# Optimization experiments

Hardware: AMD Instinct MI355X
Metric: run time of the kernel (lower is better)

The kernel has to match this reference:

```python
import jax, jax.numpy as jnp
import numpy as np

N_ATOMS = 50000
N_EDGES = 800000
EMB = 128      # emb_size_atom
EMB_BF = 128   # emb_size_bf
N_HIDDEN = 3
INV_SQRT2 = 0.7071067811865476
SILU_SCALE = 1.0 / 0.6  # GemNet ScaledSiLU


def scaled_silu(x):
    return jax.nn.silu(x) * SILU_SCALE


def residual_layer(x, w0, w1):
    # ResidualLayer(units, nLayers=2): two bias-free Dense+ScaledSiLU, then inv_sqrt(2)*(x + y)
    y = scaled_silu(x @ w0)
    y = scaled_silu(y @ w1)
    return (x + y) * INV_SQRT2


def setup_inputs() -> dict:
    key = jax.random.key(0)
    ks = jax.random.split(key, 9)
    s_emb = 1.0 / np.float32(np.sqrt(EMB))
    s_bf = 1.0 / np.float32(np.sqrt(EMB_BF))
    return {
        "h": jax.random.normal(ks[0], (N_ATOMS, EMB), jnp.float32),
        "bf": jax.random.uniform(ks[1], (N_EDGES, EMB_BF), jnp.float32),
        "idx_s": jax.random.randint(ks[2], (N_EDGES,), 0, N_ATOMS, jnp.int64),
        "idx_t": jax.random.randint(ks[3], (N_EDGES,), 0, N_ATOMS, jnp.int64),
        "w_bf": jax.random.normal(ks[4], (EMB_BF, EMB), jnp.float32) * s_bf,
        "w_pre": jax.random.normal(ks[5], (2, EMB, EMB), jnp.float32) * s_emb,
        "w_mlp1": jax.random.normal(ks[6], (EMB, EMB), jnp.float32) * s_emb,
        "w_res": jax.random.normal(ks[7], (N_HIDDEN, 2, EMB, EMB), jnp.float32) * s_emb,
        "scale_sum": jnp.ones((1,), jnp.float32),  # ScalingFactor (1.0 without scale_file)
    }


def reference(h, bf, idx_s, idx_t, w_bf, w_pre, w_mlp1, w_res, scale_sum):
    # pre_residual
    h_res = residual_layer(h, w_pre[0], w_pre[1])          # (nAtoms, EMB)
    # dense_bf: bias-free linear, no activation
    mlp_bf = bf @ w_bf                                     # (nEdges, EMB)
    # gather source embeddings, Hadamard multiply with edge features
    x = h_res[idx_s] * mlp_bf                              # (nEdges, EMB)
    # scatter-sum over target atoms
    x2 = jax.ops.segment_sum(x, idx_t, num_segments=N_ATOMS)  # (nAtoms, EMB)
    x = x2 * scale_sum[0]
    # MLP: Dense+activation, then nHidden residual blocks
    x = scaled_silu(x @ w_mlp1)
    for i in range(N_HIDDEN):
        x = residual_layer(x, w_res[i, 0], w_res[i, 1])
    return x
```

## Files before the change

### kernel.cpp

```cpp
#include <hip/hip_runtime.h>

#define EMB 128
#define NATOMS 50000
#define NEDGES 800000
#define PADN 50176

typedef __attribute__((ext_vector_type(8))) short bf16x8;
typedef __attribute__((ext_vector_type(4))) float f32x4;
typedef __attribute__((ext_vector_type(4))) unsigned short u16x4;

static const size_t H_RES_OFF  = 0;
static const size_t X2_OFF     = (size_t)NATOMS * EMB * 2;
static const size_t W_OFF      = X2_OFF + (size_t)NATOMS * EMB * 4;
static const size_t FLAG_OFF   = W_OFF + 10 * 128 * 128 * 2;
static const size_t COUNTS_OFF = (FLAG_OFF + 4 + 255) & ~(size_t)255;
static const size_t SEG_OFF    = COUNTS_OFF + (size_t)PADN * 4;
static const size_t CURSOR_OFF = SEG_OFF + (size_t)PADN * 4;
static const size_t BSUM_OFF   = CURSOR_OFF + (size_t)PADN * 4;
static const size_t RECS_OFF   = (BSUM_OFF + 1024 + 255) & ~(size_t)255;

__device__ __forceinline__ short f2bf(float f) {
  unsigned u = __float_as_uint(f);
  u += 0x7fffu + ((u >> 16) & 1u);
  return (short)(u >> 16);
}

__device__ __forceinline__ float bf2f(unsigned short u) {
  return __uint_as_float((unsigned)u << 16);
}

__device__ __forceinline__ float ssilu(float x) {
  return x * (1.0f / 0.6f) / (1.0f + __expf(-x));
}

__device__ __forceinline__ int xidx(int row, int k) {
  return (row << 7) + ((((k >> 2) ^ (row & 7)) << 2) | (k & 3));
}
__device__ __forceinline__ int bidx(int row, int k) {
  return (row << 7) + ((((k >> 3) ^ (row & 7)) << 3) | (k & 7));
}

__device__ __forceinline__ void stage_w(const short* __restrict__ src, short* dst) {
  const int wave = threadIdx.x >> 6;
  const int lane = threadIdx.x & 63;
  const char* s = (const char*)src;
  char* d = (char*)dst;
#pragma unroll
  for (int i = 0; i < 8; ++i) {
    const int off = wave * 8192 + i * 1024;
    __builtin_amdgcn_global_load_lds(
        (const __attribute__((address_space(1))) void*)(s + off + lane * 16),
        (__attribute__((address_space(3))) void*)(d + off), 16, 0, 0);
  }
}

__device__ __forceinline__ void stage_x(const float* __restrict__ src, int row0, float* x) {
#pragma unroll
  for (int i = 0; i < 8; ++i) {
    const int c = threadIdx.x + i * 256;
    const int row = c >> 5, unit = c & 31;
    f32x4 v = {0.f, 0.f, 0.f, 0.f};
    if (row0 + row < NATOMS) v = *(const f32x4*)(src + (size_t)(row0 + row) * EMB + unit * 4);
    *(f32x4*)&x[(row << 7) + ((unit ^ (row & 7)) << 2)] = v;
  }
}

template <bool SRC_BF16>
__device__ __forceinline__ void gemm_stage(const float* xsrc, const short* ysrc,
                                           const short* w, int wr0, int lr, int lh,
                                           f32x4* acc) {
#pragma unroll
  for (int kk = 0; kk < 4; ++kk) {
    const int k0 = kk * 32 + lh * 8;
    const int ra = wr0 + lr;
    bf16x8 a;
    if constexpr (SRC_BF16) {
      a = *(const bf16x8*)&ysrc[bidx(ra, k0)];
    } else {
      f32x4 u0 = *(const f32x4*)&xsrc[xidx(ra, k0)];
      f32x4 u1 = *(const f32x4*)&xsrc[xidx(ra, k0 + 4)];
      a[0] = f2bf(u0[0]); a[1] = f2bf(u0[1]); a[2] = f2bf(u0[2]); a[3] = f2bf(u0[3]);
      a[4] = f2bf(u1[0]); a[5] = f2bf(u1[1]); a[6] = f2bf(u1[2]); a[7] = f2bf(u1[3]);
    }
#pragma unroll
    for (int j0 = 0; j0 < 8; ++j0) {
      bf16x8 b = *(const bf16x8*)&w[bidx(j0 * 16 + lr, k0)];
      acc[j0] = __builtin_amdgcn_mfma_f32_16x16x32_bf16(a, b, acc[j0], 0, 0, 0);
    }
  }
}

__global__ void prep_weights(const float* __restrict__ wbf, const float* __restrict__ wpre,
                             const float* __restrict__ wmlp1, const float* __restrict__ wres,
                             short* __restrict__ W) {
  const int s = blockIdx.x >> 7;
  const int k = blockIdx.x & 127;
  const int n = threadIdx.x;
  const float* src;
  if (s == 0) src = wbf;
  else if (s <= 2) src = wpre + (s - 1) * 16384;
  else if (s == 3) src = wmlp1;
  else src = wres + (s - 4) * 16384;
  const float v = src[k * EMB + n];
  W[s * 16384 + (n << 7) + ((((k >> 3) ^ (n & 7)) << 3) | (k & 7))] = f2bf(v);
}

__global__ void zero_ws(float* __restrict__ x2, float* __restrict__ counts) {
  const f32x4 z = {0.f, 0.f, 0.f, 0.f};
  const int stride = gridDim.x * 256;
  const int nx = NATOMS * EMB / 4;
  for (int v = blockIdx.x * 256 + threadIdx.x; v < nx; v += stride)
    *(f32x4*)(x2 + 4 * (size_t)v) = z;
  const int nc = PADN / 4;
  for (int v = blockIdx.x * 256 + threadIdx.x; v < nc; v += stride)
    *(f32x4*)(counts + 4 * (size_t)v) = z;
}

__global__ void detect_idx(const int* __restrict__ idx, int* __restrict__ flag) {
  const int lane = threadIdx.x & 63;
  const int v = idx[2 * lane + 1];
  const unsigned long long nz = __ballot(v != 0);
  if (lane == 0) *flag = (nz == 0ull) ? 1 : 0;
}

__device__ __forceinline__ int load_idx(const void* p, int e, int f64) {
  return f64 ? (int)((const long long*)p)[e] : ((const int*)p)[e];
}

__global__ void hist_kernel(const void* __restrict__ idx_t_p, int* __restrict__ counts,
                            const int* __restrict__ flag) {
  const int e = blockIdx.x * 256 + threadIdx.x;
  if (e < NEDGES) atomicAdd(&counts[load_idx(idx_t_p, e, *flag)], 1);
}

__global__ void scan_blocks(const int* __restrict__ counts, int* __restrict__ seg,
                            int* __restrict__ bsum) {
  const int i = blockIdx.x * 256 + threadIdx.x;
  const int lane = threadIdx.x & 63, wave = threadIdx.x >> 6;
  const int v = counts[i];
  int incl = v;
#pragma unroll
  for (int d = 1; d < 64; d <<= 1) {
    int t = __shfl_up(incl, d, 64);
    if (lane >= d) incl += t;
  }
  __shared__ int wtot[4];
  if (lane == 63) wtot[wave] = incl;
  __syncthreads();
  int woff = 0;
  for (int w = 0; w < wave; ++w) woff += wtot[w];
  seg[i] = woff + incl - v;
  if (threadIdx.x == 255) bsum[blockIdx.x] = woff + incl;
}

__global__ void scan_top(int* __restrict__ bsum) {
  const int i = threadIdx.x;
  const int lane = i & 63, wave = i >> 6;
  const int v = (i < 196) ? bsum[i] : 0;
  int incl = v;
#pragma unroll
  for (int d = 1; d < 64; d <<= 1) {
    int t = __shfl_up(incl, d, 64);
    if (lane >= d) incl += t;
  }
  __shared__ int wtot[4];
  if (lane == 63) wtot[wave] = incl;
  __syncthreads();
  int woff = 0;
  for (int w = 0; w < wave; ++w) woff += wtot[w];
  if (i < 196) bsum[i] = woff + incl - v;
}

__global__ void add_off(int* __restrict__ seg, const int* __restrict__ bsum,
                        int* __restrict__ cursor) {
  const int i = blockIdx.x * 256 + threadIdx.x;
  const int s = seg[i] + bsum[blockIdx.x];
  seg[i] = s;
  cursor[i] = s;
}

__global__ void scatter_kernel(const void* __restrict__ idx_s_p, const void* __restrict__ idx_t_p,
                               int* __restrict__ cursor, int4* __restrict__ recs,
                               const int* __restrict__ flag) {
  const int e = blockIdx.x * 256 + threadIdx.x;
  if (e < NEDGES) {
    const int f64 = *flag;
    const int t = load_idx(idx_t_p, e, f64);
    const int s = load_idx(idx_s_p, e, f64);
    const int pos = atomicAdd(&cursor[t], 1);
    recs[pos] = make_int4(e, s, t, 0);
  }
}

__global__ __launch_bounds__(256, 2) void atom_pre(const float* __restrict__ h,
                                                   unsigned short* __restrict__ h_res,
                                                   const short* __restrict__ W) {
  __shared__ float x_lds[64 * 128];
  __shared__ short y_lds[64 * 128];
  __shared__ short w_lds[128 * 128];
  const int lane = threadIdx.x & 63, wave = threadIdx.x >> 6;
  const int lr = lane & 15, lh = lane >> 4;
  const int row0 = blockIdx.x * 64, wr0 = wave * 16;
  const f32x4 vzero = {0.f, 0.f, 0.f, 0.f};

  stage_x(h, row0, x_lds);
  stage_w(W + 1 * 16384, w_lds);
  __syncthreads();

  f32x4 acc[8];
#pragma unroll
  for (int j = 0; j < 8; ++j) acc[j] = vzero;
  gemm_stage<false>(x_lds, nullptr, w_lds, wr0, lr, lh, acc);
#pragma unroll
  for (int j0 = 0; j0 < 8; ++j0)
#pragma unroll
    for (int j = 0; j < 4; ++j)
      y_lds[bidx(wr0 + lh * 4 + j, j0 * 16 + lr)] = f2bf(ssilu(acc[j0][j]));

  __syncthreads();
  stage_w(W + 2 * 16384, w_lds);
  __syncthreads();

#pragma unroll
  for (int j = 0; j < 8; ++j) acc[j] = vzero;
  gemm_stage<true>(nullptr, y_lds, w_lds, wr0, lr, lh, acc);

#pragma unroll
  for (int j = 0; j < 4; ++j) {
    const int row = wr0 + lh * 4 + j;
    const int ga = row0 + row;
    if (ga < NATOMS) {
#pragma unroll
      for (int j0 = 0; j0 < 8; ++j0) {
        const int col = j0 * 16 + lr;
        h_res[(size_t)ga * EMB + col] = (unsigned short)f2bf(
            (x_lds[xidx(row, col)] + ssilu(acc[j0][j])) * 0.70710678118654752440f);
      }
    }
  }
}

__global__ __launch_bounds__(256, 4) void edge_swapped(const float* __restrict__ bf,
                                                       const unsigned short* __restrict__ h_res,
                                                       const int4* __restrict__ recs,
                                                       const short* __restrict__ W,
                                                       float* __restrict__ x2) {
  __shared__ short w_lds[128 * 128];
  const int lane = threadIdx.x & 63, wave = threadIdx.x >> 6;
  const int lr = lane & 15, lh = lane >> 4;

  stage_w(W, w_lds);

  const int p0 = blockIdx.x * 128 + wave * 32;
  const int4 rec = recs[p0 + (lane & 31)];
  const int it_mine = rec.z;

  const int eB0 = __shfl(rec.x, lr, 64);
  const int eB1 = __shfl(rec.x, 16 + lr, 64);
  const int isE0 = __shfl(rec.y, lr, 64);
  const int isE1 = __shfl(rec.y, 16 + lr, 64);

  __syncthreads();

  bf16x8 b_all[2][4];
#pragma unroll
  for (int kk = 0; kk < 4; ++kk) {
#pragma unroll
    for (int rf = 0; rf < 2; ++rf) {
      const int e = rf ? eB1 : eB0;
      const f32x4* p = (const f32x4*)(bf + (size_t)e * EMB + kk * 32 + lh * 8);
      f32x4 u0 = __builtin_nontemporal_load(p);
      f32x4 u1 = __builtin_nontemporal_load(p + 1);
      bf16x8 b;
      b[0] = f2bf(u0[0]); b[1] = f2bf(u0[1]); b[2] = f2bf(u0[2]); b[3] = f2bf(u0[3]);
      b[4] = f2bf(u1[0]); b[5] = f2bf(u1[1]); b[6] = f2bf(u1[2]); b[7] = f2bf(u1[3]);
      b_all[rf][kk] = b;
    }
  }

  const f32x4 vzero = {0.f, 0.f, 0.f, 0.f};

#pragma unroll 1
  for (int hf = 0; hf < 2; ++hf) {
    f32x4 acc[2][4];
#pragma unroll
    for (int rf = 0; rf < 2; ++rf)
#pragma unroll
      for (int q = 0; q < 4; ++q) acc[rf][q] = vzero;

#pragma unroll
    for (int kk = 0; kk < 4; ++kk) {
#pragma unroll
      for (int q = 0; q < 4; ++q) {
        bf16x8 a = *(const bf16x8*)&w_lds[bidx((4 * hf + q) * 16 + lr, kk * 32 + lh * 8)];
        acc[0][q] = __builtin_amdgcn_mfma_f32_16x16x32_bf16(a, b_all[0][kk], acc[0][q], 0, 0, 0);
        acc[1][q] = __builtin_amdgcn_mfma_f32_16x16x32_bf16(a, b_all[1][kk], acc[1][q], 0, 0, 0);
      }
    }

#pragma unroll
    for (int rf = 0; rf < 2; ++rf) {
      const unsigned short* hr = h_res + (size_t)(rf ? isE1 : isE0) * EMB + 4 * lh;
#pragma unroll
      for (int q = 0; q < 4; ++q) {
        u16x4 hv = *(const u16x4*)(hr + 16 * (4 * hf + q));
#pragma unroll
        for (int j = 0; j < 4; ++j) acc[rf][q][j] *= bf2f(hv[j]);
      }
    }

    int r = 0;
    while (r < 32) {
      const int t = __shfl(it_mine, r, 64);
      const unsigned long long bal = __ballot(it_mine == t);
      const unsigned long long m = (bal & 0xffffffffull) >> r;
      const int cnt = (int)__builtin_ctzll(~m);
      const int end = r + cnt;

      float v[4][4];
      const bool in0 = (lr >= r) && (lr < end);
      const bool in1 = (lr + 16 >= r) && (lr + 16 < end);
#pragma unroll
      for (int q = 0; q < 4; ++q)
#pragma unroll
        for (int j = 0; j < 4; ++j) {
          float s = 0.f;
          if (in0) s += acc[0][q][j];
          if (in1) s += acc[1][q][j];
          v[q][j] = s;
        }
#pragma unroll
      for (int d = 1; d < 16; d <<= 1)
#pragma unroll
        for (int q = 0; q < 4; ++q)
#pragma unroll
          for (int j = 0; j < 4; ++j)
            v[q][j] += __shfl_xor(v[q][j], d, 64);

      const bool interior = (r > 0) && (end < 32);
      if (lr == 0) {
        float* orow = x2 + (size_t)t * EMB + 4 * lh;
        if (interior) {
#pragma unroll
          for (int q = 0; q < 4; ++q) {
            f32x4 o = {v[q][0], v[q][1], v[q][2], v[q][3]};
            *(f32x4*)(orow + 16 * (4 * hf + q)) = o;
          }
        } else {
#pragma unroll
          for (int q = 0; q < 4; ++q)
#pragma unroll
            for (int j = 0; j < 4; ++j)
              atomicAdd(&orow[16 * (4 * hf + q) + j], v[q][j]);
        }
      }
      r = end;
    }
  }
}

__global__ __launch_bounds__(256, 2) void atom_post(const float* __restrict__ x2,
                                                    float* __restrict__ out,
                                                    const short* __restrict__ W,
                                                    const float* __restrict__ scale_sum) {
  __shared__ float x_lds[64 * 128];
  __shared__ short y_lds[64 * 128];
  __shared__ short w_lds[128 * 128];
  const int lane = threadIdx.x & 63, wave = threadIdx.x >> 6;
  const int lr = lane & 15, lh = lane >> 4;
  const int row0 = blockIdx.x * 64, wr0 = wave * 16;
  const float sc = scale_sum[0];
  const f32x4 vzero = {0.f, 0.f, 0.f, 0.f};

  stage_x(x2, row0, x_lds);
  stage_w(W + 3 * 16384, w_lds);
  __syncthreads();

  f32x4 acc[8];
#pragma unroll
  for (int j = 0; j < 8; ++j) acc[j] = vzero;
  gemm_stage<false>(x_lds, nullptr, w_lds, wr0, lr, lh, acc);
#pragma unroll
  for (int j0 = 0; j0 < 8; ++j0)
#pragma unroll
    for (int j = 0; j < 4; ++j)
      x_lds[xidx(wr0 + lh * 4 + j, j0 * 16 + lr)] = ssilu(acc[j0][j] * sc);

  for (int L = 0; L < 3; ++L) {
    __syncthreads();
    stage_w(W + (size_t)(4 + 2 * L) * 16384, w_lds);
    __syncthreads();
#pragma unroll
    for (int j = 0; j < 8; ++j) acc[j] = vzero;
    gemm_stage<false>(x_lds, nullptr, w_lds, wr0, lr, lh, acc);
#pragma unroll
    for (int j0 = 0; j0 < 8; ++j0)
#pragma unroll
      for (int j = 0; j < 4; ++j)
        y_lds[bidx(wr0 + lh * 4 + j, j0 * 16 + lr)] = f2bf(ssilu(acc[j0][j]));

    __syncthreads();
    stage_w(W + (size_t)(5 + 2 * L) * 16384, w_lds);
    __syncthreads();
#pragma unroll
    for (int j = 0; j < 8; ++j) acc[j] = vzero;
    gemm_stage<true>(nullptr, y_lds, w_lds, wr0, lr, lh, acc);

    if (L < 2) {
#pragma unroll
      for (int j = 0; j < 4; ++j) {
        const int row = wr0 + lh * 4 + j;
#pragma unroll
        for (int j0 = 0; j0 < 8; ++j0) {
          const int col = j0 * 16 + lr;
          const float xv = x_lds[xidx(row, col)];
          x_lds[xidx(row, col)] = (xv + ssilu(acc[j0][j])) * 0.70710678118654752440f;
        }
      }
    } else {
#pragma unroll
      for (int j = 0; j < 4; ++j) {
        const int row = wr0 + lh * 4 + j;
        const int ga = row0 + row;
        if (ga < NATOMS) {
#pragma unroll
          for (int j0 = 0; j0 < 8; ++j0) {
            const int col = j0 * 16 + lr;
            out[(size_t)ga * EMB + col] =
                (x_lds[xidx(row, col)] + ssilu(acc[j0][j])) * 0.70710678118654752440f;
          }
        }
      }
    }
  }
}

extern "C" void kernel_launch(void* const* d_in, const int* in_sizes, int n_in,
                              void* d_out, int out_size, void* d_ws, size_t ws_size,
                              hipStream_t stream) {
  const float* h      = (const float*)d_in[0];
  const float* bf     = (const float*)d_in[1];
  const void*  idx_s  = d_in[2];
  const void*  idx_t  = d_in[3];
  const float* w_bf   = (const float*)d_in[4];
  const float* w_pre  = (const float*)d_in[5];
  const float* w_mlp1 = (const float*)d_in[6];
  const float* w_res  = (const float*)d_in[7];
  const float* scale  = (const float*)d_in[8];
  float* out = (float*)d_out;

  char* ws = (char*)d_ws;
  unsigned short* h_res = (unsigned short*)(ws + H_RES_OFF);
  float* x2     = (float*)(ws + X2_OFF);
  short* W      = (short*)(ws + W_OFF);
  int*   flag   = (int*)(ws + FLAG_OFF);
  int*   counts = (int*)(ws + COUNTS_OFF);
  int*   segp   = (int*)(ws + SEG_OFF);
  int*   cursor = (int*)(ws + CURSOR_OFF);
  int*   bsum   = (int*)(ws + BSUM_OFF);
  int4*  recs   = (int4*)(ws + RECS_OFF);

  zero_ws<<<dim3(1024), dim3(256), 0, stream>>>(x2, (float*)counts);
  prep_weights<<<dim3(10 * 128), dim3(128), 0, stream>>>(w_bf, w_pre, w_mlp1, w_res, W);
  detect_idx<<<dim3(1), dim3(64), 0, stream>>>((const int*)idx_s, flag);

  hist_kernel<<<dim3(NEDGES / 256), dim3(256), 0, stream>>>(idx_t, counts, flag);
  scan_blocks<<<dim3(PADN / 256), dim3(256), 0, stream>>>(counts, segp, bsum);
  scan_top<<<dim3(1), dim3(256), 0, stream>>>(bsum);
  add_off<<<dim3(PADN / 256), dim3(256), 0, stream>>>(segp, bsum, cursor);
  scatter_kernel<<<dim3(NEDGES / 256), dim3(256), 0, stream>>>(idx_s, idx_t, cursor, recs, flag);

  atom_pre<<<dim3((NATOMS + 63) / 64), dim3(256), 0, stream>>>(h, h_res, W);
  edge_swapped<<<dim3(NEDGES / 128), dim3(256), 0, stream>>>(bf, h_res, recs, W, x2);
  atom_post<<<dim3((NATOMS + 63) / 64), dim3(256), 0, stream>>>(x2, out, W, scale);
}
```

Measured before the change: 366.9 us.

## Pack edge records to 8 bytes, read weights from global, prefetch h_res gathers

Edge records shrink from int4 to uint2 by packing source and target atom indices into 16 bits each, halving record traffic in the scatter and edge kernels. The edge kernel no longer stages the 128x128 weight tile into LDS or synchronises, and instead reads fragments directly from global memory, relying on cache. The h_res gathers are hoisted ahead of the MFMA loop to overlap their latency, and the half loop is fully unrolled. Register pressure rises and weight reads now depend on L1/L2 hit rates rather than LDS.

```diff
diff --git a/kernel.cpp b/kernel.cpp
--- a/kernel.cpp
+++ b/kernel.cpp
@@ -180,7 +180,7 @@
 }
 
 __global__ void scatter_kernel(const void* __restrict__ idx_s_p, const void* __restrict__ idx_t_p,
-                               int* __restrict__ cursor, int4* __restrict__ recs,
+                               int* __restrict__ cursor, uint2* __restrict__ recs,
                                const int* __restrict__ flag) {
   const int e = blockIdx.x * 256 + threadIdx.x;
   if (e < NEDGES) {
@@ -188,7 +188,7 @@
     const int t = load_idx(idx_t_p, e, f64);
     const int s = load_idx(idx_s_p, e, f64);
     const int pos = atomicAdd(&cursor[t], 1);
-    recs[pos] = make_int4(e, s, t, 0);
+    recs[pos] = make_uint2((unsigned)e, (unsigned)s | ((unsigned)t << 16));
   }
 }
 
@@ -240,27 +240,35 @@
   }
 }
 
-__global__ __launch_bounds__(256, 4) void edge_swapped(const float* __restrict__ bf,
-                                                       const unsigned short* __restrict__ h_res,
-                                                       const int4* __restrict__ recs,
-                                                       const short* __restrict__ W,
-                                                       float* __restrict__ x2) {
-  __shared__ short w_lds[128 * 128];
-  const int lane = threadIdx.x & 63, wave = threadIdx.x >> 6;
+__global__ __launch_bounds__(256) void edge_swapped(const float* __restrict__ bf,
+                                                    const unsigned short* __restrict__ h_res,
+                                                    const uint2* __restrict__ recs,
+                                                    const short* __restrict__ W,
+                                                    float* __restrict__ x2) {
+  const int lane = threadIdx.x & 63;
+  const int wave = threadIdx.x >> 6;
   const int lr = lane & 15, lh = lane >> 4;
 
-  stage_w(W, w_lds);
-
   const int p0 = blockIdx.x * 128 + wave * 32;
-  const int4 rec = recs[p0 + (lane & 31)];
-  const int it_mine = rec.z;
-
-  const int eB0 = __shfl(rec.x, lr, 64);
-  const int eB1 = __shfl(rec.x, 16 + lr, 64);
-  const int isE0 = __shfl(rec.y, lr, 64);
-  const int isE1 = __shfl(rec.y, 16 + lr, 64);
-
-  __syncthreads();
+  const uint2 rec = recs[p0 + (lane & 31)];
+  const int it_mine = (int)(rec.y >> 16);
+  const int is_mine = (int)(rec.y & 0xffffu);
+
+  const int eB0 = __shfl((int)rec.x, lr, 64);
+  const int eB1 = __shfl((int)rec.x, 16 + lr, 64);
+  const int isE0 = __shfl(is_mine, lr, 64);
+  const int isE1 = __shfl(is_mine, 16 + lr, 64);
+
+  u16x4 hv[2][2][4];
+#pragma unroll
+  for (int rf = 0; rf < 2; ++rf) {
+    const unsigned short* hr = h_res + (size_t)(rf ? isE1 : isE0) * EMB + 4 * lh;
+#pragma unroll
+    for (int hf = 0; hf < 2; ++hf)
+#pragma unroll
+      for (int q = 0; q < 4; ++q)
+        hv[rf][hf][q] = *(const u16x4*)(hr + 16 * (4 * hf + q));
+  }
 
   bf16x8 b_all[2][4];
 #pragma unroll
@@ -280,7 +288,7 @@
 
   const f32x4 vzero = {0.f, 0.f, 0.f, 0.f};
 
-#pragma unroll 1
+#pragma unroll
   for (int hf = 0; hf < 2; ++hf) {
     f32x4 acc[2][4];
 #pragma unroll
@@ -292,22 +300,19 @@
     for (int kk = 0; kk < 4; ++kk) {
 #pragma unroll
       for (int q = 0; q < 4; ++q) {
-        bf16x8 a = *(const bf16x8*)&w_lds[bidx((4 * hf + q) * 16 + lr, kk * 32 + lh * 8)];
+        bf16x8 a = *(const bf16x8*)&W[bidx((4 * hf + q) * 16 + lr, kk * 32 + lh * 8)];
         acc[0][q] = __builtin_amdgcn_mfma_f32_16x16x32_bf16(a, b_all[0][kk], acc[0][q], 0, 0, 0);
         acc[1][q] = __builtin_amdgcn_mfma_f32_16x16x32_bf16(a, b_all[1][kk], acc[1][q], 0, 0, 0);
       }
     }
 
 #pragma unroll
-    for (int rf = 0; rf < 2; ++rf) {
-      const unsigned short* hr = h_res + (size_t)(rf ? isE1 : isE0) * EMB + 4 * lh;
-#pragma unroll
-      for (int q = 0; q < 4; ++q) {
-        u16x4 hv = *(const u16x4*)(hr + 16 * (4 * hf + q));
-#pragma unroll
-        for (int j = 0; j < 4; ++j) acc[rf][q][j] *= bf2f(hv[j]);
-      }
-    }
+    for (int rf = 0; rf < 2; ++rf)
+#pragma unroll
+      for (int q = 0; q < 4; ++q)
+#pragma unroll
+        for (int j = 0; j < 4; ++j)
+          acc[rf][q][j] *= bf2f(hv[rf][hf][q][j]);
 
     int r = 0;
     while (r < 32) {
@@ -458,7 +463,7 @@
   int*   segp   = (int*)(ws + SEG_OFF);
   int*   cursor = (int*)(ws + CURSOR_OFF);
   int*   bsum   = (int*)(ws + BSUM_OFF);
-  int4*  recs   = (int4*)(ws + RECS_OFF);
+  uint2* recs   = (uint2*)(ws + RECS_OFF);
 
   zero_ws<<<dim3(1024), dim3(256), 0, stream>>>(x2, (float*)counts);
   prep_weights<<<dim3(10 * 128), dim3(128), 0, stream>>>(w_bf, w_pre, w_mlp1, w_res, W);
```

Measured after the change: 408.3 us. 11.3% more time.

## Split edge kernel into coalesced GEMM with sorted bf16 scatter and segment reduce

Applied to the files above, without the earlier changes.

The fused edge kernel, which gathered bf rows in sorted-target order, is split in two. A GEMM kernel reads bf coalesced in original edge order and writes bf16 results to their sorted positions through a per-edge rank array. A separate kernel then does the h_res gather, the multiply and the segmented reduction over contiguous sorted rows. Edge records are also packed into 32-bit words. This trades the scattered fp32 bf reads for an extra bf16 intermediate written and read back (about 200MB) plus a second launch.

```diff
diff --git a/kernel.cpp b/kernel.cpp
--- a/kernel.cpp
+++ b/kernel.cpp
@@ -8,6 +8,7 @@
 typedef __attribute__((ext_vector_type(8))) short bf16x8;
 typedef __attribute__((ext_vector_type(4))) float f32x4;
 typedef __attribute__((ext_vector_type(4))) unsigned short u16x4;
+typedef __attribute__((ext_vector_type(8))) unsigned short u16x8;
 
 static const size_t H_RES_OFF  = 0;
 static const size_t X2_OFF     = (size_t)NATOMS * EMB * 2;
@@ -17,7 +18,9 @@
 static const size_t SEG_OFF    = COUNTS_OFF + (size_t)PADN * 4;
 static const size_t CURSOR_OFF = SEG_OFF + (size_t)PADN * 4;
 static const size_t BSUM_OFF   = CURSOR_OFF + (size_t)PADN * 4;
-static const size_t RECS_OFF   = (BSUM_OFF + 1024 + 255) & ~(size_t)255;
+static const size_t RANK_OFF   = (BSUM_OFF + 1024 + 255) & ~(size_t)255;
+static const size_t RECS_OFF   = RANK_OFF + (size_t)NEDGES * 4;
+static const size_t MLP_OFF    = (RECS_OFF + (size_t)NEDGES * 4 + 255) & ~(size_t)255;
 
 __device__ __forceinline__ short f2bf(float f) {
   unsigned u = __float_as_uint(f);
@@ -180,15 +183,16 @@
 }
 
 __global__ void scatter_kernel(const void* __restrict__ idx_s_p, const void* __restrict__ idx_t_p,
-                               int* __restrict__ cursor, int4* __restrict__ recs,
-                               const int* __restrict__ flag) {
+                               int* __restrict__ cursor, int* __restrict__ rank,
+                               unsigned* __restrict__ recs, const int* __restrict__ flag) {
   const int e = blockIdx.x * 256 + threadIdx.x;
   if (e < NEDGES) {
     const int f64 = *flag;
     const int t = load_idx(idx_t_p, e, f64);
     const int s = load_idx(idx_s_p, e, f64);
     const int pos = atomicAdd(&cursor[t], 1);
-    recs[pos] = make_int4(e, s, t, 0);
+    rank[e] = pos;
+    recs[pos] = (unsigned)s | ((unsigned)t << 16);
   }
 }
 
@@ -240,35 +244,26 @@
   }
 }
 
-__global__ __launch_bounds__(256, 4) void edge_swapped(const float* __restrict__ bf,
-                                                       const unsigned short* __restrict__ h_res,
-                                                       const int4* __restrict__ recs,
-                                                       const short* __restrict__ W,
-                                                       float* __restrict__ x2) {
+__global__ __launch_bounds__(256, 2) void mlp_gemm(const float* __restrict__ bf,
+                                                   const int* __restrict__ rank,
+                                                   const short* __restrict__ W,
+                                                   unsigned short* __restrict__ mlp_s) {
   __shared__ short w_lds[128 * 128];
-  const int lane = threadIdx.x & 63, wave = threadIdx.x >> 6;
+  __shared__ unsigned short tile[128 * 128];
+  const int tid = threadIdx.x;
+  const int lane = tid & 63, wave = tid >> 6;
   const int lr = lane & 15, lh = lane >> 4;
+  const int ebase = blockIdx.x * 128;
+  const int e0 = ebase + wave * 32;
 
   stage_w(W, w_lds);
 
-  const int p0 = blockIdx.x * 128 + wave * 32;
-  const int4 rec = recs[p0 + (lane & 31)];
-  const int it_mine = rec.z;
-
-  const int eB0 = __shfl(rec.x, lr, 64);
-  const int eB1 = __shfl(rec.x, 16 + lr, 64);
-  const int isE0 = __shfl(rec.y, lr, 64);
-  const int isE1 = __shfl(rec.y, 16 + lr, 64);
-
-  __syncthreads();
-
   bf16x8 b_all[2][4];
 #pragma unroll
   for (int kk = 0; kk < 4; ++kk) {
 #pragma unroll
     for (int rf = 0; rf < 2; ++rf) {
-      const int e = rf ? eB1 : eB0;
-      const f32x4* p = (const f32x4*)(bf + (size_t)e * EMB + kk * 32 + lh * 8);
+      const f32x4* p = (const f32x4*)(bf + (size_t)(e0 + rf * 16 + lr) * EMB + kk * 32 + lh * 8);
       f32x4 u0 = __builtin_nontemporal_load(p);
       f32x4 u1 = __builtin_nontemporal_load(p + 1);
       bf16x8 b;
@@ -278,9 +273,10 @@
     }
   }
 
+  __syncthreads();
+
   const f32x4 vzero = {0.f, 0.f, 0.f, 0.f};
-
-#pragma unroll 1
+#pragma unroll
   for (int hf = 0; hf < 2; ++hf) {
     f32x4 acc[2][4];
 #pragma unroll
@@ -300,63 +296,109 @@
 
 #pragma unroll
     for (int rf = 0; rf < 2; ++rf) {
-      const unsigned short* hr = h_res + (size_t)(rf ? isE1 : isE0) * EMB + 4 * lh;
 #pragma unroll
       for (int q = 0; q < 4; ++q) {
-        u16x4 hv = *(const u16x4*)(hr + 16 * (4 * hf + q));
-#pragma unroll
-        for (int j = 0; j < 4; ++j) acc[rf][q][j] *= bf2f(hv[j]);
+        const int row = wave * 32 + rf * 16 + lr;
+        const int n0 = (4 * hf + q) * 16 + 4 * lh;
+        u16x4 pk;
+        pk[0] = (unsigned short)f2bf(acc[rf][q][0]);
+        pk[1] = (unsigned short)f2bf(acc[rf][q][1]);
+        pk[2] = (unsigned short)f2bf(acc[rf][q][2]);
+        pk[3] = (unsigned short)f2bf(acc[rf][q][3]);
+        *(u16x4*)&tile[(row << 7) + ((((n0 >> 3) ^ (row & 7)) << 3) | (n0 & 7))] = pk;
       }
     }
-
-    int r = 0;
-    while (r < 32) {
-      const int t = __shfl(it_mine, r, 64);
-      const unsigned long long bal = __ballot(it_mine == t);
-      const unsigned long long m = (bal & 0xffffffffull) >> r;
-      const int cnt = (int)__builtin_ctzll(~m);
-      const int end = r + cnt;
-
-      float v[4][4];
-      const bool in0 = (lr >= r) && (lr < end);
-      const bool in1 = (lr + 16 >= r) && (lr + 16 < end);
-#pragma unroll
-      for (int q = 0; q < 4; ++q)
-#pragma unroll
-        for (int j = 0; j < 4; ++j) {
-          float s = 0.f;
-          if (in0) s += acc[0][q][j];
-          if (in1) s += acc[1][q][j];
-          v[q][j] = s;
+  }
+
+  __syncthreads();
+
+#pragma unroll
+  for (int it = 0; it < 8; ++it) {
+    const int row = it * 16 + (tid >> 4);
+    const int unit = tid & 15;
+    const int pos = rank[ebase + row];
+    u16x8 v = *(const u16x8*)&tile[(row << 7) + ((unit ^ (row & 7)) << 3)];
+    __builtin_nontemporal_store(v, (u16x8*)(mlp_s + (size_t)pos * EMB + unit * 8));
+  }
+}
+
+__device__ __forceinline__ void seg_flush(float (&acc)[8], int t, bool interior,
+                                          float* __restrict__ x2, int lr, int lh) {
+#pragma unroll
+  for (int i = 0; i < 8; ++i) {
+    acc[i] += __shfl_xor(acc[i], 16, 64);
+    acc[i] += __shfl_xor(acc[i], 32, 64);
+  }
+  if (lh == 0) {
+    float* orow = x2 + (size_t)t * EMB + lr * 8;
+    if (interior) {
+      f32x4 a = {acc[0], acc[1], acc[2], acc[3]};
+      f32x4 b = {acc[4], acc[5], acc[6], acc[7]};
+      *(f32x4*)orow = a;
+      *(f32x4*)(orow + 4) = b;
+    } else {
+#pragma unroll
+      for (int i = 0; i < 8; ++i) atomicAdd(&orow[i], acc[i]);
+    }
+  }
+}
+
+__global__ __launch_bounds__(256, 4) void reduce_seg(const unsigned short* __restrict__ mlp_s,
+                                                     const unsigned short* __restrict__ h_res,
+                                                     const unsigned* __restrict__ recs,
+                                                     float* __restrict__ x2) {
+  const int lane = threadIdx.x & 63;
+  const int wave = threadIdx.x >> 6;
+  const int lr = lane & 15, lh = lane >> 4;
+  const int p0 = blockIdx.x * 128 + wave * 32;
+
+  const unsigned rec_mine = recs[p0 + (lane & 31)];
+
+  u16x8 m8[8], h8[8];
+  int t_my[8];
+#pragma unroll
+  for (int g = 0; g < 8; ++g) {
+    const unsigned rec = (unsigned)__shfl((int)rec_mine, g * 4 + lh, 64);
+    t_my[g] = (int)(rec >> 16);
+    const int is_g = (int)(rec & 0xffffu);
+    m8[g] = *(const u16x8*)(mlp_s + (size_t)(p0 + g * 4 + lh) * EMB + lr * 8);
+    h8[g] = *(const u16x8*)(h_res + (size_t)is_g * EMB + lr * 8);
+  }
+
+  float acc[8];
+#pragma unroll
+  for (int i = 0; i < 8; ++i) acc[i] = 0.f;
+  int t_cur = __shfl(t_my[0], 0, 64);
+  int run_start = 0;
+
+#pragma unroll
+  for (int g = 0; g < 8; ++g) {
+    float prod[8];
+#pragma unroll
+    for (int i = 0; i < 8; ++i) prod[i] = bf2f(m8[g][i]) * bf2f(h8[g][i]);
+
+    if (__all(t_my[g] == t_cur)) {
+#pragma unroll
+      for (int i = 0; i < 8; ++i) acc[i] += prod[i];
+    } else {
+#pragma unroll
+      for (int r = 0; r < 4; ++r) {
+        const int t_r = __shfl(t_my[g], r << 4, 64);
+        if (t_r != t_cur) {
+          seg_flush(acc, t_cur, run_start > 0, x2, lr, lh);
+          t_cur = t_r;
+          run_start = g * 4 + r;
+#pragma unroll
+          for (int i = 0; i < 8; ++i) acc[i] = 0.f;
         }
-#pragma unroll
-      for (int d = 1; d < 16; d <<= 1)
-#pragma unroll
-        for (int q = 0; q < 4; ++q)
-#pragma unroll
-          for (int j = 0; j < 4; ++j)
-            v[q][j] += __shfl_xor(v[q][j], d, 64);
-
-      const bool interior = (r > 0) && (end < 32);
-      if (lr == 0) {
-        float* orow = x2 + (size_t)t * EMB + 4 * lh;
-        if (interior) {
-#pragma unroll
-          for (int q = 0; q < 4; ++q) {
-            f32x4 o = {v[q][0], v[q][1], v[q][2], v[q][3]};
-            *(f32x4*)(orow + 16 * (4 * hf + q)) = o;
-          }
-        } else {
-#pragma unroll
-          for (int q = 0; q < 4; ++q)
-#pragma unroll
-            for (int j = 0; j < 4; ++j)
-              atomicAdd(&orow[16 * (4 * hf + q) + j], v[q][j]);
+        if (lh == r) {
+#pragma unroll
+          for (int i = 0; i < 8; ++i) acc[i] += prod[i];
         }
       }
-      r = end;
-    }
-  }
+    }
+  }
+  seg_flush(acc, t_cur, false, x2, lr, lh);
 }
 
 __global__ __launch_bounds__(256, 2) void atom_post(const float* __restrict__ x2,
@@ -458,7 +500,9 @@
   int*   segp   = (int*)(ws + SEG_OFF);
   int*   cursor = (int*)(ws + CURSOR_OFF);
   int*   bsum   = (int*)(ws + BSUM_OFF);
-  int4*  recs   = (int4*)(ws + RECS_OFF);
+  int*   rank   = (int*)(ws + RANK_OFF);
+  unsigned* recs = (unsigned*)(ws + RECS_OFF);
+  unsigned short* mlp_s = (unsigned short*)(ws + MLP_OFF);
 
   zero_ws<<<dim3(1024), dim3(256), 0, stream>>>(x2, (float*)counts);
   prep_weights<<<dim3(10 * 128), dim3(128), 0, stream>>>(w_bf, w_pre, w_mlp1, w_res, W);
@@ -468,9 +512,11 @@
   scan_blocks<<<dim3(PADN / 256), dim3(256), 0, stream>>>(counts, segp, bsum);
   scan_top<<<dim3(1), dim3(256), 0, stream>>>(bsum);
   add_off<<<dim3(PADN / 256), dim3(256), 0, stream>>>(segp, bsum, cursor);
-  scatter_kernel<<<dim3(NEDGES / 256), dim3(256), 0, stream>>>(idx_s, idx_t, cursor, recs, flag);
+  scatter_kernel<<<dim3(NEDGES / 256), dim3(256), 0, stream>>>(idx_s, idx_t, cursor, rank,
+                                                               recs, flag);
 
   atom_pre<<<dim3((NATOMS + 63) / 64), dim3(256), 0, stream>>>(h, h_res, W);
-  edge_swapped<<<dim3(NEDGES / 128), dim3(256), 0, stream>>>(bf, h_res, recs, W, x2);
+  mlp_gemm<<<dim3(NEDGES / 128), dim3(256), 0, stream>>>(bf, rank, W, mlp_s);
+  reduce_seg<<<dim3(NEDGES / 128), dim3(256), 0, stream>>>(mlp_s, h_res, recs, x2);
   atom_post<<<dim3((NATOMS + 63) / 64), dim3(256), 0, stream>>>(x2, out, W, scale);
 }
```

After: 541.4 us (median of 2 runs). +47.5%, slower.
